# Optimization experiments

Hardware: AMD Instinct MI355X
Metric: run time of the kernel (lower is better)

## Reference

```python
import jax, jax.numpy as jnp
import numpy as np

S, B, E, NH, F = 1024, 8, 1024, 16, 4096
HD = E // NH
NEG_INF = -1e9


def layer_norm(x, g, b, eps=1e-5):
    mu = jnp.mean(x, axis=-1, keepdims=True)
    var = jnp.mean(jnp.square(x - mu), axis=-1, keepdims=True)
    return (x - mu) * jax.lax.rsqrt(var + eps) * g + b


def setup_inputs() -> dict:
    key = jax.random.key(0)
    ks = jax.random.split(key, 26)
    sE = 1.0 / np.sqrt(E)
    sF = 1.0 / np.sqrt(F)
    inp = {
        'x': jax.random.normal(ks[0], (S, B, E), jnp.float32),
        'z': jax.random.normal(ks[1], (1, B, E), jnp.float32),
        # self-attention (torch Linear convention: weight is (out,in))
        'wq': jax.random.normal(ks[2], (E, E), jnp.float32) * sE,
        'bq': jnp.zeros((E,), jnp.float32),
        'wk': jax.random.normal(ks[3], (E, E), jnp.float32) * sE,
        'bk': jnp.zeros((E,), jnp.float32),
        'wv': jax.random.normal(ks[4], (E, E), jnp.float32) * sE,
        'bv': jnp.zeros((E,), jnp.float32),
        'wo': jax.random.normal(ks[5], (E, E), jnp.float32) * sE,
        'bo': jnp.zeros((E,), jnp.float32),
        'ln1_g': jnp.ones((E,), jnp.float32),
        'ln1_b': jnp.zeros((E,), jnp.float32),
        # gated fusion block
        'pgh_w': jax.random.normal(ks[6], (E, E), jnp.float32) * sE,
        'pgh_b': jnp.zeros((E,), jnp.float32),
        'pgz_w': jax.random.normal(ks[7], (E, E), jnp.float32) * sE,
        'pgz_b': jnp.zeros((E,), jnp.float32),
        'pv_w': jax.random.normal(ks[8], (E, E), jnp.float32) * sE,
        'pv_b': jnp.zeros((E,), jnp.float32),
        'ln2_g': jnp.ones((E,), jnp.float32),
        'ln2_b': jnp.zeros((E,), jnp.float32),
        # FFN
        'fc1_w': jax.random.normal(ks[9], (F, E), jnp.float32) * sE,
        'fc1_b': jnp.zeros((F,), jnp.float32),
        'fc2_w': jax.random.normal(ks[10], (E, F), jnp.float32) * sF,
        'fc2_b': jnp.zeros((E,), jnp.float32),
        'ln3_g': jnp.ones((E,), jnp.float32),
        'ln3_b': jnp.zeros((E,), jnp.float32),
    }
    return inp


def _forward(x, z, wq, bq, wk, bk, wv, bv, wo, bo, ln1_g, ln1_b,
             pgh_w, pgh_b, pgz_w, pgz_b, pv_w, pv_b, ln2_g, ln2_b,
             fc1_w, fc1_b, fc2_w, fc2_b, ln3_g, ln3_b):
    # ---- self attention (post-LN, causal decoder mask) ----
    residual = x
    scale = 1.0 / np.sqrt(HD)
    q = (x @ wq.T + bq) * scale          # (S,B,E)
    k = x @ wk.T + bk
    v = x @ wv.T + bv
    # (S,B,E) -> (B,NH,S,HD)
    def split_heads(t):
        return t.reshape(S, B, NH, HD).transpose(1, 2, 0, 3)
    qh, kh, vh = split_heads(q), split_heads(k), split_heads(v)
    scores = jnp.einsum('bhqd,bhkd->bhqk', qh, kh)
    causal = jnp.tril(jnp.ones((S, S), bool))
    scores = jnp.where(causal, scores, NEG_INF)
    probs = jax.nn.softmax(scores, axis=-1)
    attn_out = jnp.einsum('bhqk,bhkd->bhqd', probs, vh)  # (B,NH,S,HD)
    attn_out = attn_out.transpose(2, 0, 1, 3).reshape(S, B, E)
    attn_out = attn_out @ wo.T + bo
    x = layer_norm(residual + attn_out, ln1_g, ln1_b)
    # ---- gated fusion with bottleneck ----
    residual = x
    zb = jnp.broadcast_to(z, (S, B, E))
    gate = jax.nn.sigmoid((x @ pgh_w.T + pgh_b) + (zb @ pgz_w.T + pgz_b))
    fused = gate * (zb @ pv_w.T + pv_b)
    x = layer_norm(residual + fused, ln2_g, ln2_b)
    # ---- FFN ----
    residual = x
    h = jax.nn.relu(x @ fc1_w.T + fc1_b)
    ff = h @ fc2_w.T + fc2_b
    x = layer_norm(residual + ff, ln3_g, ln3_b)
    return x


def reference(x, z, wq, bq, wk, bk, wv, bv, wo, bo, ln1_g, ln1_b,
              pgh_w, pgh_b, pgz_w, pgz_b, pv_w, pv_b, ln2_g, ln2_b,
              fc1_w, fc1_b, fc2_w, fc2_b, ln3_g, ln3_b):
    return _forward(x, z, wq, bq, wk, bk, wv, bv, wo, bo, ln1_g, ln1_b,
                    pgh_w, pgh_b, pgz_w, pgz_b, pv_w, pv_b, ln2_g, ln2_b,
                    fc1_w, fc1_b, fc2_w, fc2_b, ln3_g, ln3_b)
```

## Files before the change

kernel.cpp:

```cpp
#include <hip/hip_runtime.h>
#include <stdint.h>
#include <stddef.h>

#define S_LEN 1024
#define BATCH 8
#define EMB   1024
#define NHEAD 16
#define HDIM  64
#define FDIM  4096
#define NTOK  (S_LEN*BATCH)

typedef unsigned short u16s;
typedef __attribute__((ext_vector_type(4))) float  f32x4;
typedef __attribute__((ext_vector_type(8))) u16s   u16x8;
typedef __attribute__((ext_vector_type(4))) u16s   u16x4;
typedef __attribute__((ext_vector_type(8))) __bf16 bf16x8;

__device__ __forceinline__ u16s f2bf(float f) {
  unsigned int x = __float_as_uint(f);
  return (u16s)((x + 0x7FFFu + ((x >> 16) & 1u)) >> 16);
}
__device__ __forceinline__ float bf2f(u16s u) {
  return __uint_as_float((unsigned int)u << 16);
}

__device__ __forceinline__ f32x4 mfma_bf16(u16x8 a, u16x8 b, f32x4 c) {
  return __builtin_amdgcn_mfma_f32_16x16x32_bf16(
      __builtin_bit_cast(bf16x8, a), __builtin_bit_cast(bf16x8, b), c, 0, 0, 0);
}

__device__ __forceinline__ void gload16(const void* g, void* l) {
  __builtin_amdgcn_global_load_lds(
      (const __attribute__((address_space(1))) unsigned int*)g,
      (__attribute__((address_space(3))) unsigned int*)l, 16, 0, 0);
}

__global__ __launch_bounds__(256) void prep_kernel(
    const float* __restrict__ x, const float* __restrict__ wq,
    const float* __restrict__ wk, const float* __restrict__ wv,
    const float* __restrict__ wo, const float* __restrict__ pghw,
    const float* __restrict__ fc1w, const float* __restrict__ fc2w,
    u16s* __restrict__ xb, u16s* __restrict__ bw_qkv, u16s* __restrict__ bw_o,
    u16s* __restrict__ bw_g, u16s* __restrict__ bw_f1, u16s* __restrict__ bw_f2) {
  const int b = blockIdx.x;
  const float* src; u16s* dst; int base;
  if (b < 8192)       { src = x;    dst = xb;                base = 0; }
  else if (b < 9216)  { src = wq;   dst = bw_qkv;            base = 8192; }
  else if (b < 10240) { src = wk;   dst = bw_qkv + 1048576;  base = 9216; }
  else if (b < 11264) { src = wv;   dst = bw_qkv + 2097152;  base = 10240; }
  else if (b < 12288) { src = wo;   dst = bw_o;              base = 11264; }
  else if (b < 13312) { src = pghw; dst = bw_g;              base = 12288; }
  else if (b < 17408) { src = fc1w; dst = bw_f1;             base = 13312; }
  else                { src = fc2w; dst = bw_f2;             base = 17408; }
  const int i = (b - base) * 256 + threadIdx.x;
  float4 v = ((const float4*)src)[i];
  u16x4 o;
  o[0] = f2bf(v.x); o[1] = f2bf(v.y); o[2] = f2bf(v.z); o[3] = f2bf(v.w);
  ((u16x4*)dst)[i] = o;
}

__global__ __launch_bounds__(256) void small_kernel(
    const float* __restrict__ z,
    const float* __restrict__ pgzw, const float* __restrict__ pgzb,
    const float* __restrict__ pvw,  const float* __restrict__ pvb,
    float* __restrict__ zgb, float* __restrict__ zvb,
    const float* __restrict__ bq, const float* __restrict__ bk,
    const float* __restrict__ bv, float* __restrict__ bqkv) {
  const int blk = blockIdx.x;
  if (blk < 512) {
    const int wid = threadIdx.x >> 6, lane = threadIdx.x & 63;
    const int idx = blk * 4 + wid;
    const int which = idx >> 10, o = idx & 1023;
    const float* w    = which ? pvw : pgzw;
    const float* bias = which ? pvb : pgzb;
    float* out        = which ? zvb : zgb;
    const float* wr = w + (size_t)o * EMB + lane * 16;
    float wv[16];
#pragma unroll
    for (int c = 0; c < 4; ++c) {
      float4 t = *(const float4*)(wr + c * 4);
      wv[c * 4 + 0] = t.x; wv[c * 4 + 1] = t.y; wv[c * 4 + 2] = t.z; wv[c * 4 + 3] = t.w;
    }
    float acc[8];
#pragma unroll
    for (int b = 0; b < 8; ++b) {
      const float* zr = z + b * EMB + lane * 16;
      float s = 0.f;
#pragma unroll
      for (int c = 0; c < 4; ++c) {
        float4 t = *(const float4*)(zr + c * 4);
        s += t.x * wv[c * 4 + 0] + t.y * wv[c * 4 + 1] +
             t.z * wv[c * 4 + 2] + t.w * wv[c * 4 + 3];
      }
      acc[b] = s;
    }
#pragma unroll
    for (int m = 1; m < 64; m <<= 1)
#pragma unroll
      for (int b = 0; b < 8; ++b) acc[b] += __shfl_xor(acc[b], m);
    if (lane < 8) out[lane * EMB + o] = acc[lane] + bias[o];
  } else {
    const int i = (blk - 512) * 256 + threadIdx.x;
    bqkv[i] = (i < 1024) ? bq[i] : (i < 2048) ? bk[i - 1024] : bv[i - 2048];
  }
}

template <int MODE>
__global__ __launch_bounds__(256) void ln_kernel(const u16s* __restrict__ y,
                                                 const float* __restrict__ gam,
                                                 const float* __restrict__ bet,
                                                 u16s* __restrict__ obf,
                                                 float* __restrict__ of) {
  const int row = blockIdx.x;
  const int t = threadIdx.x;
  const u16s* yr = y + (size_t)row * EMB;
  u16x4 raw = ((const u16x4*)yr)[t];
  float4 v;
  v.x = bf2f(raw[0]); v.y = bf2f(raw[1]); v.z = bf2f(raw[2]); v.w = bf2f(raw[3]);
  float s = v.x + v.y + v.z + v.w;
  float s2 = v.x * v.x + v.y * v.y + v.z * v.z + v.w * v.w;
#pragma unroll
  for (int m = 1; m < 64; m <<= 1) { s += __shfl_xor(s, m); s2 += __shfl_xor(s2, m); }
  __shared__ float red[8];
  const int wid = t >> 6, lane = t & 63;
  if (lane == 0) { red[wid] = s; red[4 + wid] = s2; }
  __syncthreads();
  s = red[0] + red[1] + red[2] + red[3];
  s2 = red[4] + red[5] + red[6] + red[7];
  float mu = s * (1.f / EMB);
  float var = s2 * (1.f / EMB) - mu * mu;
  float rs = rsqrtf(var + 1e-5f);
  float4 g = ((const float4*)gam)[t];
  float4 b = ((const float4*)bet)[t];
  float4 o;
  o.x = (v.x - mu) * rs * g.x + b.x;
  o.y = (v.y - mu) * rs * g.y + b.y;
  o.z = (v.z - mu) * rs * g.z + b.z;
  o.w = (v.w - mu) * rs * g.w + b.w;
  if constexpr (MODE == 0) {
    u16x4 p;
    p[0] = f2bf(o.x); p[1] = f2bf(o.y); p[2] = f2bf(o.z); p[3] = f2bf(o.w);
    ((u16x4*)(obf + (size_t)row * EMB))[t] = p;
  } else {
    ((float4*)(of + (size_t)row * EMB))[t] = o;
  }
}

enum { EPI_QKV3 = 0, EPI_RELU = 1, EPI_RES = 2, EPI_GATE = 3 };

template <int EPI>
__global__ __launch_bounds__(256, 4) void gemm_nt(const u16s* __restrict__ A,
                                                  const u16s* __restrict__ Bw,
                                                  const float* __restrict__ bias,
                                                  void* __restrict__ out,
                                                  const u16s* __restrict__ res,
                                                  const float* __restrict__ zg,
                                                  const float* __restrict__ zv,
                                                  int M, int N, int K, float scale) {
  __shared__ u16s As[128 * 64];
  __shared__ u16s Bs[128 * 64];
  const int tid = threadIdx.x;
  const int wid = tid >> 6, lane = tid & 63;
  const int wm = wid >> 1, wn = wid & 1;
  const int l15 = lane & 15, l4 = lane >> 4;

  const int nwg = gridDim.x * gridDim.y;
  int lin = blockIdx.y * gridDim.x + blockIdx.x;
  lin = (lin & 7) * (nwg >> 3) + (lin >> 3);
  const int bn0 = (lin % gridDim.x) * 128;
  const int bm0 = (lin / gridDim.x) * 128;

  const int wbase = tid & ~63;
  int srowA[4], scolA[4];
#pragma unroll
  for (int ii = 0; ii < 4; ++ii) {
    const int ell = ii * 256 + tid;
    const int row = ell >> 3;
    srowA[ii] = row;
    scolA[ii] = ((ell & 7) ^ (row & 7)) * 8;
  }

  f32x4 acc[4][4] = {};
  const int nkt = K >> 6;
  for (int kt = 0; kt < nkt; ++kt) {
#pragma unroll
    for (int ii = 0; ii < 4; ++ii) {
      gload16(A + (size_t)(bm0 + srowA[ii]) * K + kt * 64 + scolA[ii],
              As + (size_t)(ii * 256 + wbase) * 8);
      gload16(Bw + (size_t)(bn0 + srowA[ii]) * K + kt * 64 + scolA[ii],
              Bs + (size_t)(ii * 256 + wbase) * 8);
    }
    __syncthreads();
#pragma unroll
    for (int kk = 0; kk < 2; ++kk) {
      const int cs = kk * 4 + l4;
      u16x8 af[4], bfr[4];
#pragma unroll
      for (int i = 0; i < 4; ++i) {
        const int row = wm * 64 + i * 16 + l15;
        af[i] = *(const u16x8*)(As + row * 64 + (cs ^ (l15 & 7)) * 8);
      }
#pragma unroll
      for (int j = 0; j < 4; ++j) {
        const int row = wn * 64 + j * 16 + l15;
        bfr[j] = *(const u16x8*)(Bs + row * 64 + (cs ^ (l15 & 7)) * 8);
      }
      __builtin_amdgcn_s_setprio(1);
#pragma unroll
      for (int i = 0; i < 4; ++i)
#pragma unroll
        for (int j = 0; j < 4; ++j)
          acc[i][j] = mfma_bf16(bfr[j], af[i], acc[i][j]);
      __builtin_amdgcn_s_setprio(0);
    }
    __syncthreads();
  }

  u16s* outb = (u16s*)out;
#pragma unroll
  for (int i = 0; i < 4; ++i) {
    const int gr = bm0 + wm * 64 + i * 16 + l15;
#pragma unroll
    for (int j = 0; j < 4; ++j) {
      const int gc0 = bn0 + wn * 64 + j * 16 + l4 * 4;
      const float4 bv = *(const float4*)(bias + gc0);
      float v0 = acc[i][j][0] + bv.x, v1 = acc[i][j][1] + bv.y;
      float v2 = acc[i][j][2] + bv.z, v3 = acc[i][j][3] + bv.w;
      if constexpr (EPI == EPI_QKV3) {
        const int which = gc0 >> 10, col0 = gc0 & 1023;
        const int srow = gr >> 3, b = gr & 7, h = col0 >> 6, d0 = col0 & 63;
        if (which == 0) {
          u16x4 p; p[0] = f2bf(v0 * scale); p[1] = f2bf(v1 * scale);
          p[2] = f2bf(v2 * scale); p[3] = f2bf(v3 * scale);
          *(u16x4*)(outb + (size_t)(b * 16 + h) * 65536 + srow * 64 + d0) = p;
        } else if (which == 1) {
          u16x4 p; p[0] = f2bf(v0); p[1] = f2bf(v1); p[2] = f2bf(v2); p[3] = f2bf(v3);
          *(u16x4*)(outb + 8388608 + (size_t)(b * 16 + h) * 65536 + srow * 64 + d0) = p;
        } else {
          outb[16777216 + ((size_t)(b * 16 + h) * 64 + d0 + 0) * 1024 + srow] = f2bf(v0);
          outb[16777216 + ((size_t)(b * 16 + h) * 64 + d0 + 1) * 1024 + srow] = f2bf(v1);
          outb[16777216 + ((size_t)(b * 16 + h) * 64 + d0 + 2) * 1024 + srow] = f2bf(v2);
          outb[16777216 + ((size_t)(b * 16 + h) * 64 + d0 + 3) * 1024 + srow] = f2bf(v3);
        }
      } else if constexpr (EPI == EPI_RELU) {
        u16x4 p; p[0] = f2bf(fmaxf(v0, 0.f)); p[1] = f2bf(fmaxf(v1, 0.f));
        p[2] = f2bf(fmaxf(v2, 0.f)); p[3] = f2bf(fmaxf(v3, 0.f));
        *(u16x4*)(outb + (size_t)gr * N + gc0) = p;
      } else if constexpr (EPI == EPI_RES) {
        const u16x4 rr = *(const u16x4*)(res + (size_t)gr * N + gc0);
        u16x4 p; p[0] = f2bf(v0 + bf2f(rr[0])); p[1] = f2bf(v1 + bf2f(rr[1]));
        p[2] = f2bf(v2 + bf2f(rr[2])); p[3] = f2bf(v3 + bf2f(rr[3]));
        *(u16x4*)(outb + (size_t)gr * N + gc0) = p;
      } else {
        const float4 zg4 = *(const float4*)(zg + (gr & 7) * EMB + gc0);
        const float4 zv4 = *(const float4*)(zv + (gr & 7) * EMB + gc0);
        const u16x4 rr = *(const u16x4*)(res + (size_t)gr * EMB + gc0);
        u16x4 p;
        p[0] = f2bf(bf2f(rr[0]) + zv4.x / (1.f + __expf(-(v0 + zg4.x))));
        p[1] = f2bf(bf2f(rr[1]) + zv4.y / (1.f + __expf(-(v1 + zg4.y))));
        p[2] = f2bf(bf2f(rr[2]) + zv4.z / (1.f + __expf(-(v2 + zg4.z))));
        p[3] = f2bf(bf2f(rr[3]) + zv4.w / (1.f + __expf(-(v3 + zg4.w))));
        *(u16x4*)(outb + (size_t)gr * EMB + gc0) = p;
      }
    }
  }
}

__global__ __launch_bounds__(256) void attn_kernel(const u16s* __restrict__ Q,
                                                   const u16s* __restrict__ K,
                                                   const u16s* __restrict__ VT,
                                                   u16s* __restrict__ O) {
  __shared__ u16s Ks[64 * 72];
  __shared__ u16s Vs[64 * 72];
  __shared__ u16s Pl[4][16 * 72];
  const int p = blockIdx.x, bh = blockIdx.y;
  const int tid = threadIdx.x;
  const int wid = tid >> 6, lane = tid & 63;
  const int l15 = lane & 15, l4 = lane >> 4;
  const size_t hoff = (size_t)bh * (S_LEN * HDIM);
  const u16s* Qb = Q + hoff;
  const u16s* Kb = K + hoff;
  const u16s* Vb = VT + hoff;
  u16s* Pw = Pl[wid];
  const int b = bh >> 4, h = bh & 15;

  int srow[2], scol[2];
#pragma unroll
  for (int i = 0; i < 2; ++i) {
    const int ell = i * 256 + tid;
    srow[i] = ell >> 3;
    scol[i] = (ell & 7) * 8;
  }

  for (int half = 0; half < 2; ++half) {
    const int qt = half ? (15 - p) : p;
    const int qrow = qt * 64 + wid * 16 + l15;
    const u16x8 qf0 = *(const u16x8*)(Qb + qrow * 64 + l4 * 8);
    const u16x8 qf1 = *(const u16x8*)(Qb + qrow * 64 + 32 + l4 * 8);
    f32x4 oa[4] = {};
    float mrun = -1e30f, lsum = 0.f;
    const int nkt = qt + 1;

    u16x8 kreg[2], vreg[2];
#pragma unroll
    for (int i = 0; i < 2; ++i) {
      kreg[i] = *(const u16x8*)(Kb + (size_t)srow[i] * 64 + scol[i]);
      vreg[i] = *(const u16x8*)(Vb + (size_t)srow[i] * 1024 + scol[i]);
    }

    for (int kt = 0; kt < nkt; ++kt) {
      __syncthreads();
#pragma unroll
      for (int i = 0; i < 2; ++i) {
        *(u16x8*)(Ks + srow[i] * 72 + scol[i]) = kreg[i];
        *(u16x8*)(Vs + srow[i] * 72 + scol[i]) = vreg[i];
      }
      __syncthreads();
      if (kt + 1 < nkt) {
#pragma unroll
        for (int i = 0; i < 2; ++i) {
          kreg[i] = *(const u16x8*)(Kb + (size_t)((kt + 1) * 64 + srow[i]) * 64 + scol[i]);
          vreg[i] = *(const u16x8*)(Vb + (size_t)srow[i] * 1024 + (kt + 1) * 64 + scol[i]);
        }
      }
      const int kbase = kt * 64;
      f32x4 sc[4] = {};
      {
        u16x8 kfA[4], kfB[4];
#pragma unroll
        for (int g = 0; g < 4; ++g) {
          kfA[g] = *(const u16x8*)(Ks + (g * 16 + l15) * 72 + l4 * 8);
          kfB[g] = *(const u16x8*)(Ks + (g * 16 + l15) * 72 + 32 + l4 * 8);
        }
        __builtin_amdgcn_s_setprio(1);
#pragma unroll
        for (int g = 0; g < 4; ++g) {
          sc[g] = mfma_bf16(kfA[g], qf0, sc[g]);
          sc[g] = mfma_bf16(kfB[g], qf1, sc[g]);
        }
        __builtin_amdgcn_s_setprio(0);
      }
      u16x8 vf0[4], vf1[4];
#pragma unroll
      for (int df = 0; df < 4; ++df) {
        vf0[df] = *(const u16x8*)(Vs + (df * 16 + l15) * 72 + l4 * 8);
        vf1[df] = *(const u16x8*)(Vs + (df * 16 + l15) * 72 + 32 + l4 * 8);
      }

      float sv[16];
      float pmax = -1e30f;
#pragma unroll
      for (int g = 0; g < 4; ++g)
#pragma unroll
        for (int r = 0; r < 4; ++r) {
          const int kg = kbase + g * 16 + l4 * 4 + r;
          const float s0 = (kg <= qrow) ? sc[g][r] : -1e9f;
          sv[g * 4 + r] = s0;
          pmax = fmaxf(pmax, s0);
        }
      pmax = fmaxf(pmax, __shfl_xor(pmax, 16));
      pmax = fmaxf(pmax, __shfl_xor(pmax, 32));
      const float mnew = fmaxf(mrun, pmax);
      const float fsc = __expf(mrun - mnew);
      float psum = 0.f;
#pragma unroll
      for (int i = 0; i < 16; ++i) { float pv = __expf(sv[i] - mnew); sv[i] = pv; psum += pv; }
      psum += __shfl_xor(psum, 16);
      psum += __shfl_xor(psum, 32);
      lsum = lsum * fsc + psum;
      mrun = mnew;
#pragma unroll
      for (int df = 0; df < 4; ++df) oa[df] *= fsc;

#pragma unroll
      for (int g = 0; g < 4; ++g) {
        u16x4 pk;
#pragma unroll
        for (int r = 0; r < 4; ++r) pk[r] = f2bf(sv[g * 4 + r]);
        *(u16x4*)(Pw + l15 * 72 + g * 16 + l4 * 4) = pk;
      }
      asm volatile("s_waitcnt lgkmcnt(0)" ::: "memory");
      const u16x8 pf0 = *(const u16x8*)(Pw + l15 * 72 + l4 * 8);
      const u16x8 pf1 = *(const u16x8*)(Pw + l15 * 72 + 32 + l4 * 8);
      __builtin_amdgcn_s_setprio(1);
#pragma unroll
      for (int df = 0; df < 4; ++df) {
        oa[df] = mfma_bf16(vf0[df], pf0, oa[df]);
        oa[df] = mfma_bf16(vf1[df], pf1, oa[df]);
      }
      __builtin_amdgcn_s_setprio(0);
    }
    const float inv = 1.f / lsum;
    u16s* orow = O + ((size_t)qrow * 8 + b) * EMB + h * 64;
#pragma unroll
    for (int df = 0; df < 4; ++df)
#pragma unroll
      for (int r = 0; r < 4; ++r)
        orow[df * 16 + l4 * 4 + r] = f2bf(oa[df][r] * inv);
  }
}

extern "C" void kernel_launch(void* const* d_in, const int* in_sizes, int n_in,
                              void* d_out, int out_size, void* d_ws, size_t ws_size,
                              hipStream_t stream) {
  const float* x = (const float*)d_in[0];
  const float* z = (const float*)d_in[1];
  const float* wq = (const float*)d_in[2];  const float* bq = (const float*)d_in[3];
  const float* wk = (const float*)d_in[4];  const float* bk = (const float*)d_in[5];
  const float* wv = (const float*)d_in[6];  const float* bv = (const float*)d_in[7];
  const float* wo = (const float*)d_in[8];  const float* bo = (const float*)d_in[9];
  const float* ln1g = (const float*)d_in[10]; const float* ln1b = (const float*)d_in[11];
  const float* pghw = (const float*)d_in[12]; const float* pghb = (const float*)d_in[13];
  const float* pgzw = (const float*)d_in[14]; const float* pgzb = (const float*)d_in[15];
  const float* pvw  = (const float*)d_in[16]; const float* pvb  = (const float*)d_in[17];
  const float* ln2g = (const float*)d_in[18]; const float* ln2b = (const float*)d_in[19];
  const float* fc1w = (const float*)d_in[20]; const float* fc1b = (const float*)d_in[21];
  const float* fc2w = (const float*)d_in[22]; const float* fc2b = (const float*)d_in[23];
  const float* ln3g = (const float*)d_in[24]; const float* ln3b = (const float*)d_in[25];

  char* ws = (char*)d_ws;
  size_t off = 0;
  auto alloc = [&](size_t bytes) -> char* {
    char* p = ws + off;
    off += (bytes + 255) & ~(size_t)255;
    return p;
  };

  u16s* bw_qkv = (u16s*)alloc(2u * 3145728);
  u16s* bw_o = (u16s*)alloc(2u * 1048576);
  u16s* bw_g = (u16s*)alloc(2u * 1048576);
  u16s* bw_f1 = (u16s*)alloc(2u * 4194304);
  u16s* bw_f2 = (u16s*)alloc(2u * 4194304);
  u16s* xb = (u16s*)alloc(2u * 8388608);
  u16s* qh = (u16s*)alloc(2u * 8388608);
  u16s* kh = (u16s*)alloc(2u * 8388608);
  u16s* vT = (u16s*)alloc(2u * 8388608);
  u16s* attnb = (u16s*)alloc(2u * 8388608);
  u16s* hbuf = qh;
  u16s* ybufb = (u16s*)alloc(2u * 8388608);
  u16s* x1b = (u16s*)alloc(2u * 8388608);
  u16s* x2b = (u16s*)alloc(2u * 8388608);
  float* zgb = (float*)alloc(4u * 8192);
  float* zvb = (float*)alloc(4u * 8192);
  float* bqkv = (float*)alloc(4u * 3072);
  (void)off; (void)ws_size; (void)in_sizes; (void)n_in; (void)out_size;
  (void)kh; (void)vT;

  prep_kernel<<<21504, 256, 0, stream>>>(x, wq, wk, wv, wo, pghw, fc1w, fc2w,
                                         xb, bw_qkv, bw_o, bw_g, bw_f1, bw_f2);
  small_kernel<<<524, 256, 0, stream>>>(z, pgzw, pgzb, pvw, pvb, zgb, zvb,
                                        bq, bk, bv, bqkv);

  gemm_nt<EPI_QKV3><<<dim3(24, 64), 256, 0, stream>>>(
      xb, bw_qkv, bqkv, qh, nullptr, nullptr, nullptr, NTOK, 3072, EMB, 0.125f);

  attn_kernel<<<dim3(8, 128), 256, 0, stream>>>(qh, kh, vT, attnb);

  gemm_nt<EPI_RES><<<dim3(8, 64), 256, 0, stream>>>(
      attnb, bw_o, bo, ybufb, xb, nullptr, nullptr, NTOK, EMB, EMB, 1.f);
  ln_kernel<0><<<NTOK, 256, 0, stream>>>(ybufb, ln1g, ln1b, x1b, nullptr);

  gemm_nt<EPI_GATE><<<dim3(8, 64), 256, 0, stream>>>(
      x1b, bw_g, pghb, ybufb, x1b, zgb, zvb, NTOK, EMB, EMB, 1.f);
  ln_kernel<0><<<NTOK, 256, 0, stream>>>(ybufb, ln2g, ln2b, x2b, nullptr);

  gemm_nt<EPI_RELU><<<dim3(32, 64), 256, 0, stream>>>(
      x2b, bw_f1, fc1b, hbuf, nullptr, nullptr, nullptr, NTOK, FDIM, EMB, 1.f);
  gemm_nt<EPI_RES><<<dim3(8, 64), 256, 0, stream>>>(
      hbuf, bw_f2, fc2b, ybufb, x2b, nullptr, nullptr, NTOK, EMB, FDIM, 1.f);
  ln_kernel<1><<<NTOK, 256, 0, stream>>>(ybufb, ln3g, ln3b, nullptr, (float*)d_out);
}
```

Measured before the change: 437.7 us.

## Add 256x256 eight-wave pipelined GEMM for QKV and FC1 projections

Measured after the change: 443.6 us. Within noise of the previous version (+1.4%).

```diff
diff --git a/kernel.cpp b/kernel.cpp
--- a/kernel.cpp
+++ b/kernel.cpp
@@ -33,6 +33,18 @@
   __builtin_amdgcn_global_load_lds(
       (const __attribute__((address_space(1))) unsigned int*)g,
       (__attribute__((address_space(3))) unsigned int*)l, 16, 0, 0);
+}
+
+#define VMCNT(n) asm volatile("s_waitcnt vmcnt(" #n ")" ::: "memory")
+#define LGKM0()  do { asm volatile("s_waitcnt lgkmcnt(0)" ::: "memory"); \
+                      __builtin_amdgcn_sched_barrier(0); } while (0)
+
+__device__ __forceinline__ void block_sync() {
+  __builtin_amdgcn_sched_barrier(0);
+  asm volatile("" ::: "memory");
+  __builtin_amdgcn_s_barrier();
+  asm volatile("" ::: "memory");
+  __builtin_amdgcn_sched_barrier(0);
 }
 
 __global__ __launch_bounds__(256) void prep_kernel(
@@ -149,6 +161,54 @@
 enum { EPI_QKV3 = 0, EPI_RELU = 1, EPI_RES = 2, EPI_GATE = 3 };
 
 template <int EPI>
+__device__ __forceinline__ void epi_store(f32x4 a, int gr, int gc0, int N,
+                                          const float* __restrict__ bias,
+                                          u16s* __restrict__ outb,
+                                          const u16s* __restrict__ res,
+                                          const float* __restrict__ zg,
+                                          const float* __restrict__ zv,
+                                          float scale) {
+  const float4 bv = *(const float4*)(bias + gc0);
+  float v0 = a[0] + bv.x, v1 = a[1] + bv.y, v2 = a[2] + bv.z, v3 = a[3] + bv.w;
+  if constexpr (EPI == EPI_QKV3) {
+    const int which = gc0 >> 10, col0 = gc0 & 1023;
+    const int srow = gr >> 3, b = gr & 7, h = col0 >> 6, d0 = col0 & 63;
+    if (which == 0) {
+      u16x4 p; p[0] = f2bf(v0 * scale); p[1] = f2bf(v1 * scale);
+      p[2] = f2bf(v2 * scale); p[3] = f2bf(v3 * scale);
+      *(u16x4*)(outb + (size_t)(b * 16 + h) * 65536 + srow * 64 + d0) = p;
+    } else if (which == 1) {
+      u16x4 p; p[0] = f2bf(v0); p[1] = f2bf(v1); p[2] = f2bf(v2); p[3] = f2bf(v3);
+      *(u16x4*)(outb + 8388608 + (size_t)(b * 16 + h) * 65536 + srow * 64 + d0) = p;
+    } else {
+      outb[16777216 + ((size_t)(b * 16 + h) * 64 + d0 + 0) * 1024 + srow] = f2bf(v0);
+      outb[16777216 + ((size_t)(b * 16 + h) * 64 + d0 + 1) * 1024 + srow] = f2bf(v1);
+      outb[16777216 + ((size_t)(b * 16 + h) * 64 + d0 + 2) * 1024 + srow] = f2bf(v2);
+      outb[16777216 + ((size_t)(b * 16 + h) * 64 + d0 + 3) * 1024 + srow] = f2bf(v3);
+    }
+  } else if constexpr (EPI == EPI_RELU) {
+    u16x4 p; p[0] = f2bf(fmaxf(v0, 0.f)); p[1] = f2bf(fmaxf(v1, 0.f));
+    p[2] = f2bf(fmaxf(v2, 0.f)); p[3] = f2bf(fmaxf(v3, 0.f));
+    *(u16x4*)(outb + (size_t)gr * N + gc0) = p;
+  } else if constexpr (EPI == EPI_RES) {
+    const u16x4 rr = *(const u16x4*)(res + (size_t)gr * N + gc0);
+    u16x4 p; p[0] = f2bf(v0 + bf2f(rr[0])); p[1] = f2bf(v1 + bf2f(rr[1]));
+    p[2] = f2bf(v2 + bf2f(rr[2])); p[3] = f2bf(v3 + bf2f(rr[3]));
+    *(u16x4*)(outb + (size_t)gr * N + gc0) = p;
+  } else {
+    const float4 zg4 = *(const float4*)(zg + (gr & 7) * EMB + gc0);
+    const float4 zv4 = *(const float4*)(zv + (gr & 7) * EMB + gc0);
+    const u16x4 rr = *(const u16x4*)(res + (size_t)gr * EMB + gc0);
+    u16x4 p;
+    p[0] = f2bf(bf2f(rr[0]) + zv4.x / (1.f + __expf(-(v0 + zg4.x))));
+    p[1] = f2bf(bf2f(rr[1]) + zv4.y / (1.f + __expf(-(v1 + zg4.y))));
+    p[2] = f2bf(bf2f(rr[2]) + zv4.z / (1.f + __expf(-(v2 + zg4.z))));
+    p[3] = f2bf(bf2f(rr[3]) + zv4.w / (1.f + __expf(-(v3 + zg4.w))));
+    *(u16x4*)(outb + (size_t)gr * EMB + gc0) = p;
+  }
+}
+
+template <int EPI>
 __global__ __launch_bounds__(256, 4) void gemm_nt(const u16s* __restrict__ A,
                                                   const u16s* __restrict__ Bw,
                                                   const float* __restrict__ bias,
@@ -223,45 +283,160 @@
 #pragma unroll
     for (int j = 0; j < 4; ++j) {
       const int gc0 = bn0 + wn * 64 + j * 16 + l4 * 4;
-      const float4 bv = *(const float4*)(bias + gc0);
-      float v0 = acc[i][j][0] + bv.x, v1 = acc[i][j][1] + bv.y;
-      float v2 = acc[i][j][2] + bv.z, v3 = acc[i][j][3] + bv.w;
-      if constexpr (EPI == EPI_QKV3) {
-        const int which = gc0 >> 10, col0 = gc0 & 1023;
-        const int srow = gr >> 3, b = gr & 7, h = col0 >> 6, d0 = col0 & 63;
-        if (which == 0) {
-          u16x4 p; p[0] = f2bf(v0 * scale); p[1] = f2bf(v1 * scale);
-          p[2] = f2bf(v2 * scale); p[3] = f2bf(v3 * scale);
-          *(u16x4*)(outb + (size_t)(b * 16 + h) * 65536 + srow * 64 + d0) = p;
-        } else if (which == 1) {
-          u16x4 p; p[0] = f2bf(v0); p[1] = f2bf(v1); p[2] = f2bf(v2); p[3] = f2bf(v3);
-          *(u16x4*)(outb + 8388608 + (size_t)(b * 16 + h) * 65536 + srow * 64 + d0) = p;
-        } else {
-          outb[16777216 + ((size_t)(b * 16 + h) * 64 + d0 + 0) * 1024 + srow] = f2bf(v0);
-          outb[16777216 + ((size_t)(b * 16 + h) * 64 + d0 + 1) * 1024 + srow] = f2bf(v1);
-          outb[16777216 + ((size_t)(b * 16 + h) * 64 + d0 + 2) * 1024 + srow] = f2bf(v2);
-          outb[16777216 + ((size_t)(b * 16 + h) * 64 + d0 + 3) * 1024 + srow] = f2bf(v3);
-        }
-      } else if constexpr (EPI == EPI_RELU) {
-        u16x4 p; p[0] = f2bf(fmaxf(v0, 0.f)); p[1] = f2bf(fmaxf(v1, 0.f));
-        p[2] = f2bf(fmaxf(v2, 0.f)); p[3] = f2bf(fmaxf(v3, 0.f));
-        *(u16x4*)(outb + (size_t)gr * N + gc0) = p;
-      } else if constexpr (EPI == EPI_RES) {
-        const u16x4 rr = *(const u16x4*)(res + (size_t)gr * N + gc0);
-        u16x4 p; p[0] = f2bf(v0 + bf2f(rr[0])); p[1] = f2bf(v1 + bf2f(rr[1]));
-        p[2] = f2bf(v2 + bf2f(rr[2])); p[3] = f2bf(v3 + bf2f(rr[3]));
-        *(u16x4*)(outb + (size_t)gr * N + gc0) = p;
-      } else {
-        const float4 zg4 = *(const float4*)(zg + (gr & 7) * EMB + gc0);
-        const float4 zv4 = *(const float4*)(zv + (gr & 7) * EMB + gc0);
-        const u16x4 rr = *(const u16x4*)(res + (size_t)gr * EMB + gc0);
-        u16x4 p;
-        p[0] = f2bf(bf2f(rr[0]) + zv4.x / (1.f + __expf(-(v0 + zg4.x))));
-        p[1] = f2bf(bf2f(rr[1]) + zv4.y / (1.f + __expf(-(v1 + zg4.y))));
-        p[2] = f2bf(bf2f(rr[2]) + zv4.z / (1.f + __expf(-(v2 + zg4.z))));
-        p[3] = f2bf(bf2f(rr[3]) + zv4.w / (1.f + __expf(-(v3 + zg4.w))));
-        *(u16x4*)(outb + (size_t)gr * EMB + gc0) = p;
-      }
+      epi_store<EPI>(acc[i][j], gr, gc0, N, bias, outb, res, zg, zv, scale);
+    }
+  }
+}
+
+template <int EPI>
+__global__ __launch_bounds__(512, 1) void gemm8p(const u16s* __restrict__ A,
+                                                 const u16s* __restrict__ Bw,
+                                                 const float* __restrict__ bias,
+                                                 void* __restrict__ out,
+                                                 const u16s* __restrict__ res,
+                                                 const float* __restrict__ zg,
+                                                 const float* __restrict__ zv,
+                                                 int M, int N, int K, float scale) {
+  __shared__ u16s L[65536];
+  const int tid = threadIdx.x;
+  const int wid = tid >> 6, lane = tid & 63;
+  const int wm = wid >> 2, wn = wid & 3;
+  const int l15 = lane & 15, l4 = lane >> 4;
+
+  const int nwg = gridDim.x * gridDim.y;
+  int lin = blockIdx.y * gridDim.x + blockIdx.x;
+  lin = (lin & 7) * (nwg >> 3) + (lin >> 3);
+  const int bn0 = (lin % gridDim.x) * 256;
+  const int bm0 = (lin / gridDim.x) * 256;
+  const int nkt = K >> 6;
+
+  auto RB = [](int d, int which, int kh) { return ((d * 2 + which) * 2 + kh) * 8192; };
+
+  int srow[2], scol[2];
+#pragma unroll
+  for (int i = 0; i < 2; ++i) {
+    const int ell = i * 512 + tid;
+    srow[i] = ell >> 2;
+    scol[i] = ((ell & 3) ^ (srow[i] & 3)) * 8;
+  }
+  const int wbase = tid & ~63;
+
+  auto stageHalf = [&](const u16s* src, int row0, int skt, int kh, int rbase) {
+#pragma unroll
+    for (int i = 0; i < 2; ++i) {
+      gload16(src + (size_t)(row0 + srow[i]) * K + skt * 64 + kh * 32 + scol[i],
+              L + rbase + (size_t)(i * 512 + wbase) * 8);
+    }
+  };
+  auto rdA = [&](int rb, int row) {
+    return *(const u16x8*)(L + rb + row * 32 + (l4 ^ (row & 3)) * 8);
+  };
+
+  f32x4 acc[8][4] = {};
+
+  stageHalf(A,  bm0, 0, 0, RB(0, 0, 0));
+  stageHalf(Bw, bn0, 0, 0, RB(0, 1, 0));
+  stageHalf(A,  bm0, 0, 1, RB(0, 0, 1));
+  stageHalf(Bw, bn0, 0, 1, RB(0, 1, 1));
+  {
+    const int s1 = (nkt > 1) ? 1 : 0;
+    stageHalf(A,  bm0, s1, 0, RB(1, 0, 0));
+    stageHalf(Bw, bn0, s1, 0, RB(1, 1, 0));
+  }
+  VMCNT(4);
+  block_sync();
+
+  for (int t = 0; t < nkt; ++t) {
+    const int d = t & 1;
+    const int tp1 = (t + 1 < nkt) ? t + 1 : nkt - 1;
+    const int tp2 = (t + 2 < nkt) ? t + 2 : nkt - 1;
+    u16x8 bfr[4];
+    {
+      u16x8 af[4];
+#pragma unroll
+      for (int i = 0; i < 4; ++i)
+        af[i] = rdA(RB(d, 0, 0), wm * 128 + i * 16 + l15);
+#pragma unroll
+      for (int j = 0; j < 4; ++j)
+        bfr[j] = rdA(RB(d, 1, 0), wn * 64 + j * 16 + l15);
+      stageHalf(A, bm0, tp1, 1, RB(d ^ 1, 0, 1));
+      block_sync();
+      LGKM0();
+      __builtin_amdgcn_s_setprio(1);
+#pragma unroll
+      for (int i = 0; i < 4; ++i)
+#pragma unroll
+        for (int j = 0; j < 4; ++j)
+          acc[i][j] = mfma_bf16(bfr[j], af[i], acc[i][j]);
+      __builtin_amdgcn_s_setprio(0);
+      block_sync();
+    }
+    {
+      u16x8 af[4];
+#pragma unroll
+      for (int i = 0; i < 4; ++i)
+        af[i] = rdA(RB(d, 0, 0), wm * 128 + 64 + i * 16 + l15);
+      stageHalf(Bw, bn0, tp1, 1, RB(d ^ 1, 1, 1));
+      block_sync();
+      LGKM0();
+      __builtin_amdgcn_s_setprio(1);
+#pragma unroll
+      for (int i = 0; i < 4; ++i)
+#pragma unroll
+        for (int j = 0; j < 4; ++j)
+          acc[4 + i][j] = mfma_bf16(bfr[j], af[i], acc[4 + i][j]);
+      __builtin_amdgcn_s_setprio(0);
+      block_sync();
+    }
+    {
+      u16x8 af[4];
+#pragma unroll
+      for (int i = 0; i < 4; ++i)
+        af[i] = rdA(RB(d, 0, 1), wm * 128 + i * 16 + l15);
+#pragma unroll
+      for (int j = 0; j < 4; ++j)
+        bfr[j] = rdA(RB(d, 1, 1), wn * 64 + j * 16 + l15);
+      stageHalf(A, bm0, tp2, 0, RB(d, 0, 0));
+      block_sync();
+      LGKM0();
+      __builtin_amdgcn_s_setprio(1);
+#pragma unroll
+      for (int i = 0; i < 4; ++i)
+#pragma unroll
+        for (int j = 0; j < 4; ++j)
+          acc[i][j] = mfma_bf16(bfr[j], af[i], acc[i][j]);
+      __builtin_amdgcn_s_setprio(0);
+      block_sync();
+    }
+    {
+      u16x8 af[4];
+#pragma unroll
+      for (int i = 0; i < 4; ++i)
+        af[i] = rdA(RB(d, 0, 1), wm * 128 + 64 + i * 16 + l15);
+      stageHalf(Bw, bn0, tp2, 0, RB(d, 1, 0));
+      block_sync();
+      LGKM0();
+      __builtin_amdgcn_s_setprio(1);
+#pragma unroll
+      for (int i = 0; i < 4; ++i)
+#pragma unroll
+        for (int j = 0; j < 4; ++j)
+          acc[4 + i][j] = mfma_bf16(bfr[j], af[i], acc[4 + i][j]);
+      __builtin_amdgcn_s_setprio(0);
+      VMCNT(4);
+      block_sync();
+    }
+  }
+  VMCNT(0);
+
+  u16s* outb = (u16s*)out;
+#pragma unroll
+  for (int mi = 0; mi < 8; ++mi) {
+    const int gr = bm0 + wm * 128 + (mi >> 2) * 64 + (mi & 3) * 16 + l15;
+#pragma unroll
+    for (int j = 0; j < 4; ++j) {
+      const int gc0 = bn0 + wn * 64 + j * 16 + l4 * 4;
+      epi_store<EPI>(acc[mi][j], gr, gc0, N, bias, outb, res, zg, zv, scale);
     }
   }
 }
@@ -451,7 +626,7 @@
   small_kernel<<<524, 256, 0, stream>>>(z, pgzw, pgzb, pvw, pvb, zgb, zvb,
                                         bq, bk, bv, bqkv);
 
-  gemm_nt<EPI_QKV3><<<dim3(24, 64), 256, 0, stream>>>(
+  gemm8p<EPI_QKV3><<<dim3(12, 32), 512, 0, stream>>>(
       xb, bw_qkv, bqkv, qh, nullptr, nullptr, nullptr, NTOK, 3072, EMB, 0.125f);
 
   attn_kernel<<<dim3(8, 128), 256, 0, stream>>>(qh, kh, vT, attnb);
@@ -464,7 +639,7 @@
       x1b, bw_g, pghb, ybufb, x1b, zgb, zvb, NTOK, EMB, EMB, 1.f);
   ln_kernel<0><<<NTOK, 256, 0, stream>>>(ybufb, ln2g, ln2b, x2b, nullptr);
 
-  gemm_nt<EPI_RELU><<<dim3(32, 64), 256, 0, stream>>>(
+  gemm8p<EPI_RELU><<<dim3(16, 32), 512, 0, stream>>>(
       x2b, bw_f1, fc1b, hbuf, nullptr, nullptr, nullptr, NTOK, FDIM, EMB, 1.f);
   gemm_nt<EPI_RES><<<dim3(8, 64), 256, 0, stream>>>(
       hbuf, bw_f2, fc2b, ybufb, x2b, nullptr, nullptr, NTOK, EMB, FDIM, 1.f);
```

## Process both paired causal query tiles in one pass over shared K/V tiles

Applied to the files above, without the earlier changes.

Result: no change. 442.6 us (+1.1%).

```diff
diff --git a/kernel.cpp b/kernel.cpp
--- a/kernel.cpp
+++ b/kernel.cpp
@@ -149,6 +149,54 @@
 enum { EPI_QKV3 = 0, EPI_RELU = 1, EPI_RES = 2, EPI_GATE = 3 };
 
 template <int EPI>
+__device__ __forceinline__ void epi_store(f32x4 a, int gr, int gc0, int N,
+                                          const float* __restrict__ bias,
+                                          u16s* __restrict__ outb,
+                                          const u16s* __restrict__ res,
+                                          const float* __restrict__ zg,
+                                          const float* __restrict__ zv,
+                                          float scale) {
+  const float4 bv = *(const float4*)(bias + gc0);
+  float v0 = a[0] + bv.x, v1 = a[1] + bv.y, v2 = a[2] + bv.z, v3 = a[3] + bv.w;
+  if constexpr (EPI == EPI_QKV3) {
+    const int which = gc0 >> 10, col0 = gc0 & 1023;
+    const int srow = gr >> 3, b = gr & 7, h = col0 >> 6, d0 = col0 & 63;
+    if (which == 0) {
+      u16x4 p; p[0] = f2bf(v0 * scale); p[1] = f2bf(v1 * scale);
+      p[2] = f2bf(v2 * scale); p[3] = f2bf(v3 * scale);
+      *(u16x4*)(outb + (size_t)(b * 16 + h) * 65536 + srow * 64 + d0) = p;
+    } else if (which == 1) {
+      u16x4 p; p[0] = f2bf(v0); p[1] = f2bf(v1); p[2] = f2bf(v2); p[3] = f2bf(v3);
+      *(u16x4*)(outb + 8388608 + (size_t)(b * 16 + h) * 65536 + srow * 64 + d0) = p;
+    } else {
+      outb[16777216 + ((size_t)(b * 16 + h) * 64 + d0 + 0) * 1024 + srow] = f2bf(v0);
+      outb[16777216 + ((size_t)(b * 16 + h) * 64 + d0 + 1) * 1024 + srow] = f2bf(v1);
+      outb[16777216 + ((size_t)(b * 16 + h) * 64 + d0 + 2) * 1024 + srow] = f2bf(v2);
+      outb[16777216 + ((size_t)(b * 16 + h) * 64 + d0 + 3) * 1024 + srow] = f2bf(v3);
+    }
+  } else if constexpr (EPI == EPI_RELU) {
+    u16x4 p; p[0] = f2bf(fmaxf(v0, 0.f)); p[1] = f2bf(fmaxf(v1, 0.f));
+    p[2] = f2bf(fmaxf(v2, 0.f)); p[3] = f2bf(fmaxf(v3, 0.f));
+    *(u16x4*)(outb + (size_t)gr * N + gc0) = p;
+  } else if constexpr (EPI == EPI_RES) {
+    const u16x4 rr = *(const u16x4*)(res + (size_t)gr * N + gc0);
+    u16x4 p; p[0] = f2bf(v0 + bf2f(rr[0])); p[1] = f2bf(v1 + bf2f(rr[1]));
+    p[2] = f2bf(v2 + bf2f(rr[2])); p[3] = f2bf(v3 + bf2f(rr[3]));
+    *(u16x4*)(outb + (size_t)gr * N + gc0) = p;
+  } else {
+    const float4 zg4 = *(const float4*)(zg + (gr & 7) * EMB + gc0);
+    const float4 zv4 = *(const float4*)(zv + (gr & 7) * EMB + gc0);
+    const u16x4 rr = *(const u16x4*)(res + (size_t)gr * EMB + gc0);
+    u16x4 p;
+    p[0] = f2bf(bf2f(rr[0]) + zv4.x / (1.f + __expf(-(v0 + zg4.x))));
+    p[1] = f2bf(bf2f(rr[1]) + zv4.y / (1.f + __expf(-(v1 + zg4.y))));
+    p[2] = f2bf(bf2f(rr[2]) + zv4.z / (1.f + __expf(-(v2 + zg4.z))));
+    p[3] = f2bf(bf2f(rr[3]) + zv4.w / (1.f + __expf(-(v3 + zg4.w))));
+    *(u16x4*)(outb + (size_t)gr * EMB + gc0) = p;
+  }
+}
+
+template <int EPI>
 __global__ __launch_bounds__(256, 4) void gemm_nt(const u16s* __restrict__ A,
                                                   const u16s* __restrict__ Bw,
                                                   const float* __restrict__ bias,
@@ -223,45 +271,7 @@
 #pragma unroll
     for (int j = 0; j < 4; ++j) {
       const int gc0 = bn0 + wn * 64 + j * 16 + l4 * 4;
-      const float4 bv = *(const float4*)(bias + gc0);
-      float v0 = acc[i][j][0] + bv.x, v1 = acc[i][j][1] + bv.y;
-      float v2 = acc[i][j][2] + bv.z, v3 = acc[i][j][3] + bv.w;
-      if constexpr (EPI == EPI_QKV3) {
-        const int which = gc0 >> 10, col0 = gc0 & 1023;
-        const int srow = gr >> 3, b = gr & 7, h = col0 >> 6, d0 = col0 & 63;
-        if (which == 0) {
-          u16x4 p; p[0] = f2bf(v0 * scale); p[1] = f2bf(v1 * scale);
-          p[2] = f2bf(v2 * scale); p[3] = f2bf(v3 * scale);
-          *(u16x4*)(outb + (size_t)(b * 16 + h) * 65536 + srow * 64 + d0) = p;
-        } else if (which == 1) {
-          u16x4 p; p[0] = f2bf(v0); p[1] = f2bf(v1); p[2] = f2bf(v2); p[3] = f2bf(v3);
-          *(u16x4*)(outb + 8388608 + (size_t)(b * 16 + h) * 65536 + srow * 64 + d0) = p;
-        } else {
-          outb[16777216 + ((size_t)(b * 16 + h) * 64 + d0 + 0) * 1024 + srow] = f2bf(v0);
-          outb[16777216 + ((size_t)(b * 16 + h) * 64 + d0 + 1) * 1024 + srow] = f2bf(v1);
-          outb[16777216 + ((size_t)(b * 16 + h) * 64 + d0 + 2) * 1024 + srow] = f2bf(v2);
-          outb[16777216 + ((size_t)(b * 16 + h) * 64 + d0 + 3) * 1024 + srow] = f2bf(v3);
-        }
-      } else if constexpr (EPI == EPI_RELU) {
-        u16x4 p; p[0] = f2bf(fmaxf(v0, 0.f)); p[1] = f2bf(fmaxf(v1, 0.f));
-        p[2] = f2bf(fmaxf(v2, 0.f)); p[3] = f2bf(fmaxf(v3, 0.f));
-        *(u16x4*)(outb + (size_t)gr * N + gc0) = p;
-      } else if constexpr (EPI == EPI_RES) {
-        const u16x4 rr = *(const u16x4*)(res + (size_t)gr * N + gc0);
-        u16x4 p; p[0] = f2bf(v0 + bf2f(rr[0])); p[1] = f2bf(v1 + bf2f(rr[1]));
-        p[2] = f2bf(v2 + bf2f(rr[2])); p[3] = f2bf(v3 + bf2f(rr[3]));
-        *(u16x4*)(outb + (size_t)gr * N + gc0) = p;
-      } else {
-        const float4 zg4 = *(const float4*)(zg + (gr & 7) * EMB + gc0);
-        const float4 zv4 = *(const float4*)(zv + (gr & 7) * EMB + gc0);
-        const u16x4 rr = *(const u16x4*)(res + (size_t)gr * EMB + gc0);
-        u16x4 p;
-        p[0] = f2bf(bf2f(rr[0]) + zv4.x / (1.f + __expf(-(v0 + zg4.x))));
-        p[1] = f2bf(bf2f(rr[1]) + zv4.y / (1.f + __expf(-(v1 + zg4.y))));
-        p[2] = f2bf(bf2f(rr[2]) + zv4.z / (1.f + __expf(-(v2 + zg4.z))));
-        p[3] = f2bf(bf2f(rr[3]) + zv4.w / (1.f + __expf(-(v3 + zg4.w))));
-        *(u16x4*)(outb + (size_t)gr * EMB + gc0) = p;
-      }
+      epi_store<EPI>(acc[i][j], gr, gc0, N, bias, outb, res, zg, zv, scale);
     }
   }
 }
@@ -292,61 +302,66 @@
     scol[i] = (ell & 7) * 8;
   }
 
-  for (int half = 0; half < 2; ++half) {
-    const int qt = half ? (15 - p) : p;
-    const int qrow = qt * 64 + wid * 16 + l15;
-    const u16x8 qf0 = *(const u16x8*)(Qb + qrow * 64 + l4 * 8);
-    const u16x8 qf1 = *(const u16x8*)(Qb + qrow * 64 + 32 + l4 * 8);
-    f32x4 oa[4] = {};
-    float mrun = -1e30f, lsum = 0.f;
-    const int nkt = qt + 1;
-
-    u16x8 kreg[2], vreg[2];
+  const int qtA = p, qtB = 15 - p;
+  const int qrowA = qtA * 64 + wid * 16 + l15;
+  const int qrowB = qtB * 64 + wid * 16 + l15;
+  const u16x8 qfA0 = *(const u16x8*)(Qb + qrowA * 64 + l4 * 8);
+  const u16x8 qfA1 = *(const u16x8*)(Qb + qrowA * 64 + 32 + l4 * 8);
+  const u16x8 qfB0 = *(const u16x8*)(Qb + qrowB * 64 + l4 * 8);
+  const u16x8 qfB1 = *(const u16x8*)(Qb + qrowB * 64 + 32 + l4 * 8);
+  f32x4 oaA[4] = {}, oaB[4] = {};
+  float mrunA = -1e30f, lsumA = 0.f, mrunB = -1e30f, lsumB = 0.f;
+  const int nkt = qtB + 1;
+
+  u16x8 kreg[2], vreg[2];
+#pragma unroll
+  for (int i = 0; i < 2; ++i) {
+    kreg[i] = *(const u16x8*)(Kb + (size_t)srow[i] * 64 + scol[i]);
+    vreg[i] = *(const u16x8*)(Vb + (size_t)srow[i] * 1024 + scol[i]);
+  }
+
+  for (int kt = 0; kt < nkt; ++kt) {
+    __syncthreads();
 #pragma unroll
     for (int i = 0; i < 2; ++i) {
-      kreg[i] = *(const u16x8*)(Kb + (size_t)srow[i] * 64 + scol[i]);
-      vreg[i] = *(const u16x8*)(Vb + (size_t)srow[i] * 1024 + scol[i]);
-    }
-
-    for (int kt = 0; kt < nkt; ++kt) {
-      __syncthreads();
+      *(u16x8*)(Ks + srow[i] * 72 + scol[i]) = kreg[i];
+      *(u16x8*)(Vs + srow[i] * 72 + scol[i]) = vreg[i];
+    }
+    __syncthreads();
+    if (kt + 1 < nkt) {
 #pragma unroll
       for (int i = 0; i < 2; ++i) {
-        *(u16x8*)(Ks + srow[i] * 72 + scol[i]) = kreg[i];
-        *(u16x8*)(Vs + srow[i] * 72 + scol[i]) = vreg[i];
-      }
-      __syncthreads();
-      if (kt + 1 < nkt) {
-#pragma unroll
-        for (int i = 0; i < 2; ++i) {
-          kreg[i] = *(const u16x8*)(Kb + (size_t)((kt + 1) * 64 + srow[i]) * 64 + scol[i]);
-          vreg[i] = *(const u16x8*)(Vb + (size_t)srow[i] * 1024 + (kt + 1) * 64 + scol[i]);
-        }
-      }
-      const int kbase = kt * 64;
-      f32x4 sc[4] = {};
-      {
-        u16x8 kfA[4], kfB[4];
-#pragma unroll
-        for (int g = 0; g < 4; ++g) {
-          kfA[g] = *(const u16x8*)(Ks + (g * 16 + l15) * 72 + l4 * 8);
-          kfB[g] = *(const u16x8*)(Ks + (g * 16 + l15) * 72 + 32 + l4 * 8);
-        }
+        kreg[i] = *(const u16x8*)(Kb + (size_t)((kt + 1) * 64 + srow[i]) * 64 + scol[i]);
+        vreg[i] = *(const u16x8*)(Vb + (size_t)srow[i] * 1024 + (kt + 1) * 64 + scol[i]);
+      }
+    }
+    const int kbase = kt * 64;
+    const bool doA = (kt <= qtA);
+
+    f32x4 scA[4] = {}, scB[4] = {};
+    {
+#pragma unroll
+      for (int g = 0; g < 4; ++g) {
+        const u16x8 kf0 = *(const u16x8*)(Ks + (g * 16 + l15) * 72 + l4 * 8);
+        const u16x8 kf1 = *(const u16x8*)(Ks + (g * 16 + l15) * 72 + 32 + l4 * 8);
         __builtin_amdgcn_s_setprio(1);
-#pragma unroll
-        for (int g = 0; g < 4; ++g) {
-          sc[g] = mfma_bf16(kfA[g], qf0, sc[g]);
-          sc[g] = mfma_bf16(kfB[g], qf1, sc[g]);
+        scB[g] = mfma_bf16(kf0, qfB0, scB[g]);
+        scB[g] = mfma_bf16(kf1, qfB1, scB[g]);
+        if (doA) {
+          scA[g] = mfma_bf16(kf0, qfA0, scA[g]);
+          scA[g] = mfma_bf16(kf1, qfA1, scA[g]);
         }
         __builtin_amdgcn_s_setprio(0);
       }
-      u16x8 vf0[4], vf1[4];
-#pragma unroll
-      for (int df = 0; df < 4; ++df) {
-        vf0[df] = *(const u16x8*)(Vs + (df * 16 + l15) * 72 + l4 * 8);
-        vf1[df] = *(const u16x8*)(Vs + (df * 16 + l15) * 72 + 32 + l4 * 8);
-      }
-
+    }
+    u16x8 vf0[4], vf1[4];
+#pragma unroll
+    for (int df = 0; df < 4; ++df) {
+      vf0[df] = *(const u16x8*)(Vs + (df * 16 + l15) * 72 + l4 * 8);
+      vf1[df] = *(const u16x8*)(Vs + (df * 16 + l15) * 72 + 32 + l4 * 8);
+    }
+
+    {
       float sv[16];
       float pmax = -1e30f;
 #pragma unroll
@@ -354,24 +369,23 @@
 #pragma unroll
         for (int r = 0; r < 4; ++r) {
           const int kg = kbase + g * 16 + l4 * 4 + r;
-          const float s0 = (kg <= qrow) ? sc[g][r] : -1e9f;
+          const float s0 = (kg <= qrowB) ? scB[g][r] : -1e9f;
           sv[g * 4 + r] = s0;
           pmax = fmaxf(pmax, s0);
         }
       pmax = fmaxf(pmax, __shfl_xor(pmax, 16));
       pmax = fmaxf(pmax, __shfl_xor(pmax, 32));
-      const float mnew = fmaxf(mrun, pmax);
-      const float fsc = __expf(mrun - mnew);
+      const float mnew = fmaxf(mrunB, pmax);
+      const float fsc = __expf(mrunB - mnew);
       float psum = 0.f;
 #pragma unroll
       for (int i = 0; i < 16; ++i) { float pv = __expf(sv[i] - mnew); sv[i] = pv; psum += pv; }
       psum += __shfl_xor(psum, 16);
       psum += __shfl_xor(psum, 32);
-      lsum = lsum * fsc + psum;
-      mrun = mnew;
-#pragma unroll
-      for (int df = 0; df < 4; ++df) oa[df] *= fsc;
-
+      lsumB = lsumB * fsc + psum;
+      mrunB = mnew;
+#pragma unroll
+      for (int df = 0; df < 4; ++df) oaB[df] *= fsc;
 #pragma unroll
       for (int g = 0; g < 4; ++g) {
         u16x4 pk;
@@ -385,18 +399,72 @@
       __builtin_amdgcn_s_setprio(1);
 #pragma unroll
       for (int df = 0; df < 4; ++df) {
-        oa[df] = mfma_bf16(vf0[df], pf0, oa[df]);
-        oa[df] = mfma_bf16(vf1[df], pf1, oa[df]);
+        oaB[df] = mfma_bf16(vf0[df], pf0, oaB[df]);
+        oaB[df] = mfma_bf16(vf1[df], pf1, oaB[df]);
       }
       __builtin_amdgcn_s_setprio(0);
     }
-    const float inv = 1.f / lsum;
-    u16s* orow = O + ((size_t)qrow * 8 + b) * EMB + h * 64;
+    if (doA) {
+      float sv[16];
+      float pmax = -1e30f;
+#pragma unroll
+      for (int g = 0; g < 4; ++g)
+#pragma unroll
+        for (int r = 0; r < 4; ++r) {
+          const int kg = kbase + g * 16 + l4 * 4 + r;
+          const float s0 = (kg <= qrowA) ? scA[g][r] : -1e9f;
+          sv[g * 4 + r] = s0;
+          pmax = fmaxf(pmax, s0);
+        }
+      pmax = fmaxf(pmax, __shfl_xor(pmax, 16));
+      pmax = fmaxf(pmax, __shfl_xor(pmax, 32));
+      const float mnew = fmaxf(mrunA, pmax);
+      const float fsc = __expf(mrunA - mnew);
+      float psum = 0.f;
+#pragma unroll
+      for (int i = 0; i < 16; ++i) { float pv = __expf(sv[i] - mnew); sv[i] = pv; psum += pv; }
+      psum += __shfl_xor(psum, 16);
+      psum += __shfl_xor(psum, 32);
+      lsumA = lsumA * fsc + psum;
+      mrunA = mnew;
+#pragma unroll
+      for (int df = 0; df < 4; ++df) oaA[df] *= fsc;
+#pragma unroll
+      for (int g = 0; g < 4; ++g) {
+        u16x4 pk;
+#pragma unroll
+        for (int r = 0; r < 4; ++r) pk[r] = f2bf(sv[g * 4 + r]);
+        *(u16x4*)(Pw + l15 * 72 + g * 16 + l4 * 4) = pk;
+      }
+      asm volatile("s_waitcnt lgkmcnt(0)" ::: "memory");
+      const u16x8 pf0 = *(const u16x8*)(Pw + l15 * 72 + l4 * 8);
+      const u16x8 pf1 = *(const u16x8*)(Pw + l15 * 72 + 32 + l4 * 8);
+      __builtin_amdgcn_s_setprio(1);
+#pragma unroll
+      for (int df = 0; df < 4; ++df) {
+        oaA[df] = mfma_bf16(vf0[df], pf0, oaA[df]);
+        oaA[df] = mfma_bf16(vf1[df], pf1, oaA[df]);
+      }
+      __builtin_amdgcn_s_setprio(0);
+    }
+  }
+  {
+    const float inv = 1.f / lsumA;
+    u16s* orow = O + ((size_t)qrowA * 8 + b) * EMB + h * 64;
 #pragma unroll
     for (int df = 0; df < 4; ++df)
 #pragma unroll
       for (int r = 0; r < 4; ++r)
-        orow[df * 16 + l4 * 4 + r] = f2bf(oa[df][r] * inv);
+        orow[df * 16 + l4 * 4 + r] = f2bf(oaA[df][r] * inv);
+  }
+  {
+    const float inv = 1.f / lsumB;
+    u16s* orow = O + ((size_t)qrowB * 8 + b) * EMB + h * 64;
+#pragma unroll
+    for (int df = 0; df < 4; ++df)
+#pragma unroll
+      for (int r = 0; r < 4; ++r)
+        orow[df * 16 + l4 * 4 + r] = f2bf(oaB[df][r] * inv);
   }
 }
 
```
